# Kernel optimization log

Measured on AMD Instinct MI355X. Metric: run time of the kernel, lower is better.

The kernel has to match this reference:

```python
import jax, jax.numpy as jnp
import numpy as np

B, L1, L2, D1, D2, H, P = 32, 256, 64, 256, 256, 256, 128
I = D1 + D2  # gate / GRU input dim


def setup_inputs() -> dict:
    key = jax.random.key(0)
    ks = jax.random.split(key, 10)
    s = 0.05  # weight init scale
    return {
        "sequence1": jax.random.normal(ks[0], (B, L1, D1), jnp.float32),
        "sequence2": jax.random.normal(ks[1], (B, L2, D2), jnp.float32),
        "sequence1_mask": jnp.ones((B, L1), jnp.float32),
        "sequence2_mask": jnp.ones((B, L2), jnp.float32),
        "W1": jax.random.normal(ks[2], (D2, P), jnp.float32) * s,
        "W2": jax.random.normal(ks[3], (D1 + H, P), jnp.float32) * s,
        "v": jax.random.normal(ks[4], (P,), jnp.float32) * s,
        "Wg": jax.random.normal(ks[5], (I, I), jnp.float32) * s,
        "bg": jnp.zeros((I,), jnp.float32),
        "w_ih": jax.random.normal(ks[6], (3 * H, I), jnp.float32) * s,
        "w_hh": jax.random.normal(ks[7], (3 * H, H), jnp.float32) * s,
        "b_ih": jnp.zeros((3 * H,), jnp.float32),
        "b_hh": jnp.zeros((3 * H,), jnp.float32),
    }


def reference(sequence1, sequence2, sequence1_mask, sequence2_mask,
              W1, W2, v, Wg, bg, w_ih, w_hh, b_ih, b_hh):
    # Precompute sequence2 projection once: [B, L2, P]
    seq2_proj = jnp.einsum('bld,dp->blp', sequence2, W1)
    # Additive mask for softmax over L2
    neg = jnp.where(sequence2_mask > 0, 0.0, -1e9)  # [B, L2]
    xs = jnp.transpose(sequence1, (1, 0, 2))  # [L1, B, D1]

    def step(h, x_t):
        # attention: v^T tanh(W1*seq2_j + W2*[x_t; h])
        vec = jnp.concatenate([x_t, h], axis=-1)            # [B, D1+H]
        s = jnp.einsum('blp,p->bl',
                       jnp.tanh(seq2_proj + (vec @ W2)[:, None, :]), v) + neg
        w = jax.nn.softmax(s, axis=-1)                      # [B, L2]
        att = jnp.einsum('bl,bld->bd', w, sequence2)        # [B, D2]
        inp = jnp.concatenate([x_t, att], axis=-1)          # [B, I]
        # gated attention: sigmoid(Linear(inp)) * inp
        inp = jax.nn.sigmoid(inp @ Wg.T + bg) * inp
        # GRUCell (torch semantics)
        gi = inp @ w_ih.T + b_ih
        gh = h @ w_hh.T + b_hh
        ir, iz, inn = jnp.split(gi, 3, axis=-1)
        hr, hz, hn = jnp.split(gh, 3, axis=-1)
        r = jax.nn.sigmoid(ir + hr)
        z = jax.nn.sigmoid(iz + hz)
        n = jnp.tanh(inn + r * hn)
        h_new = (1.0 - z) * n + z * h
        return h_new, h_new

    h0 = jnp.zeros((sequence1.shape[0], w_hh.shape[1]), sequence1.dtype)
    _, hs = jax.lax.scan(step, h0, xs)                      # [L1, B, H]
    out = jnp.transpose(hs, (1, 0, 2)) * sequence1_mask[:, :, None]
    return out
```

## Files before the change

### kernel.cpp

```cpp
#include <hip/hip_runtime.h>

typedef _Float16 half2_v __attribute__((ext_vector_type(2)));
typedef unsigned int u32;

#define W2K_O    0
#define WHHP_O   16384
#define WIHP_O   114688
#define NPACKW   311296
#define S2P_B    1245184
#define S2T_B    1769472
#define M1_B     2818048
#define PROJX_B  4915200
#define GATEX_B  7012352
#define EXCH_B   15400960

#define SMEM_BYTES 149520

__device__ __forceinline__ float fdot2(half2_v a, half2_v b, float c) {
    return __builtin_amdgcn_fdot2(a, b, c, false);
}
__device__ __forceinline__ half2_v h2_of(u32 u) { return __builtin_bit_cast(half2_v, u); }
__device__ __forceinline__ u32 pack_h2(float a, float b) {
    half2_v r; r[0] = (_Float16)a; r[1] = (_Float16)b;
    return __builtin_bit_cast(u32, r);
}
__device__ __forceinline__ float dot4(uint4 w, uint4 a, float acc) {
    acc = fdot2(h2_of(w.x), h2_of(a.x), acc);
    acc = fdot2(h2_of(w.y), h2_of(a.y), acc);
    acc = fdot2(h2_of(w.z), h2_of(a.z), acc);
    acc = fdot2(h2_of(w.w), h2_of(a.w), acc);
    return acc;
}
__device__ __forceinline__ float fast_tanh(float x) {
    float e = __expf(2.0f * x);
    return 1.0f - 2.0f / (e + 1.0f);
}
__device__ __forceinline__ float fast_sigmoid(float x) {
    return 1.0f / (1.0f + __expf(-x));
}
__device__ __forceinline__ u32 aload(const u32* p) {
    return __hip_atomic_load(p, __ATOMIC_RELAXED, __HIP_MEMORY_SCOPE_AGENT);
}
__device__ __forceinline__ void astore(u32* p, u32 v) {
    __hip_atomic_store(p, v, __ATOMIC_RELAXED, __HIP_MEMORY_SCOPE_AGENT);
}
__device__ __forceinline__ u32 mkw(float x, u32 st) {
    unsigned short hb = __builtin_bit_cast(unsigned short, (_Float16)x);
    return (st << 16) | (u32)hb;
}
__device__ __forceinline__ float f16low(u32 v) {
    return (float)__builtin_bit_cast(_Float16, (unsigned short)(v & 0xFFFFu));
}

__global__ void prep_pack_w(const float* __restrict__ W2, const float* __restrict__ wih,
                            const float* __restrict__ whh, u32* __restrict__ ws_u) {
    int idx = blockIdx.x * 256 + threadIdx.x;
    if (idx >= NPACKW) return;
    float a, c;
    if (idx < WHHP_O) {
        int mm = idx >> 11, r = idx & 2047, p = r >> 4, kl = r & 15;
        int row = 256 + mm * 32 + 2 * kl;
        a = W2[row * 128 + p]; c = W2[(row + 1) * 128 + p];
    } else if (idx < WIHP_O) {
        int t2 = idx - WHHP_O, mm = t2 / 12288, r = t2 % 12288, o = r >> 7, k = r & 127;
        int row = (o >> 5) * 256 + mm * 32 + (o & 31);
        a = whh[row * 256 + 2 * k]; c = whh[row * 256 + 2 * k + 1];
    } else {
        int t2 = idx - WIHP_O, mm = t2 / 24576, r = t2 % 24576, o = r >> 8, k = r & 255;
        int row = (o >> 5) * 256 + mm * 32 + (o & 31);
        a = wih[row * 512 + 2 * k]; c = wih[row * 512 + 2 * k + 1];
    }
    ws_u[idx] = pack_h2(a, c);
}

__global__ void prep_s2p(const float* __restrict__ seq2, const float* __restrict__ W1,
                         _Float16* __restrict__ outh) {
    int idx = blockIdx.x * 256 + threadIdx.x;
    int p = idx & 127, j = (idx >> 7) & 63, b = idx >> 13;
    const float* s2 = seq2 + (b * 64 + j) * 256;
    float acc = 0.f;
    #pragma unroll 8
    for (int d = 0; d < 256; ++d) acc += s2[d] * W1[d * 128 + p];
    outh[idx] = (_Float16)acc;
}

__global__ void prep_s2T(const float* __restrict__ seq2, _Float16* __restrict__ dst) {
    int idx = blockIdx.x * 256 + threadIdx.x;
    int j = idx & 63, d = (idx >> 6) & 255, b = idx >> 14;
    dst[idx] = (_Float16)seq2[(b * 64 + j) * 256 + d];
}

__global__ void prep_m1(const float* __restrict__ Wg, const float* __restrict__ seq2,
                        _Float16* __restrict__ dst) {
    int idx = blockIdx.x * 256 + threadIdx.x;
    int j = idx & 63, o = (idx >> 6) & 511, b = idx >> 15;
    const float* wr = Wg + o * 512 + 256;
    const float* s2 = seq2 + (b * 64 + j) * 256;
    float acc = 0.f;
    #pragma unroll 8
    for (int d = 0; d < 256; ++d) acc += wr[d] * s2[d];
    dst[idx] = (_Float16)acc;
}

__global__ void prep_gemm(const float* __restrict__ A, const float* __restrict__ Bsrc,
                          int mode, _Float16* __restrict__ C, int N) {
    __shared__ float As[64][17];
    __shared__ float Bs[16][65];
    int r0 = blockIdx.x * 64, n0 = blockIdx.y * 64;
    int tid = threadIdx.x;
    int tr = tid >> 4, tc = tid & 15;
    float acc[4][4] = {};
    for (int k0 = 0; k0 < 256; k0 += 16) {
        #pragma unroll
        for (int i = 0; i < 4; ++i) {
            int rr = (tid >> 4) + i * 16, kk = tid & 15;
            As[rr][kk] = A[(r0 + rr) * 256 + k0 + kk];
        }
        #pragma unroll
        for (int i = 0; i < 4; ++i) {
            if (mode == 0) { int kk = (tid >> 6) + i * 4, nn = tid & 63; Bs[kk][nn] = Bsrc[(k0 + kk) * N + n0 + nn]; }
            else           { int nn = (tid >> 4) + i * 16, kk = tid & 15; Bs[kk][nn] = Bsrc[(n0 + nn) * 512 + k0 + kk]; }
        }
        __syncthreads();
        #pragma unroll
        for (int k = 0; k < 16; ++k)
            #pragma unroll
            for (int i = 0; i < 4; ++i)
                #pragma unroll
                for (int j = 0; j < 4; ++j)
                    acc[i][j] += As[tr * 4 + i][k] * Bs[k][tc * 4 + j];
        __syncthreads();
    }
    for (int i = 0; i < 4; ++i)
        for (int j = 0; j < 4; ++j)
            C[(size_t)(r0 + tr * 4 + i) * N + n0 + tc * 4 + j] = (_Float16)acc[i][j];
}

__global__ void __launch_bounds__(1024) match_rnn(
    const float* __restrict__ seq1, const float* __restrict__ mask1,
    const float* __restrict__ mask2, const float* __restrict__ v,
    const float* __restrict__ bg, const float* __restrict__ bih,
    const float* __restrict__ bhh, char* __restrict__ ws, float* __restrict__ out)
{
    const int m = blockIdx.x >> 5;
    const int b = blockIdx.x & 31;
    const int tid = threadIdx.x;

    extern __shared__ char smem[];
    u32* s_whh4 = (u32*)smem;
    u32* s_wih4 = s_whh4 + 12288;
    u32* s_w2k  = s_wih4 + 12288;
    u32* s_s2pU = s_w2k + 2176;
    u32* s_m1u  = s_s2pU + 4608;
    u32* s_s2Tu = s_m1u + 2112;
    float* s_redA = (float*)(s_s2Tu + 2112);
    float* s_redD = s_redA + 96;
    u32* s_h2u  = (u32*)(s_redD + 96);
    u32* s_ip2a = s_h2u + 160;
    u32* s_ip2b = s_ip2a + 160;
    float* s_projh = (float*)(s_ip2b + 160);
    float* s_projx = s_projh + 144;
    float* s_v   = s_projx + 144;
    float* s_w   = s_v + 144;
    float* s_neg = s_w + 64;
    float* s_gx  = s_neg + 64;
    float* s_xc  = s_gx + 64;
    float* s_bg  = s_xc + 64;
    float* s_sg  = s_bg + 64;
    float* s_attl = s_sg + 64;
    float* s_bih = s_attl + 64;
    float* s_bhh = s_bih + 96;
    float* s_hf  = s_bhh + 96;
    u32* s_hloc  = (u32*)(s_hf + 32);
    float* s_m1v = (float*)(s_hloc + 16);

    unsigned short* s_s2p  = (unsigned short*)s_s2pU;
    unsigned short* s_h2h  = (unsigned short*)s_h2u;
    unsigned short* s_ip2ah = (unsigned short*)s_ip2a;
    unsigned short* s_ip2bh = (unsigned short*)s_ip2b;

    const u32* wsrc = (const u32*)ws;

    for (int i = tid; i < 12288; i += 1024) {
        int o = i >> 7, k = i & 127, u = k >> 2;
        int du4 = ((o >> 3) * 256) + ((u & 3) * 64) + (((o & 7) << 3) | (u >> 2));
        s_whh4[du4 * 4 + (k & 3)] = wsrc[WHHP_O + m * 12288 + i];
    }
    for (int i = tid; i < 12288; i += 1024) {
        int o = i >> 7, k = i & 127, u = k >> 2;
        int du4 = ((o >> 3) * 256) + ((u & 3) * 64) + (((o & 7) << 3) | (u >> 2));
        s_wih4[du4 * 4 + (k & 3)] = wsrc[WIHP_O + m * 24576 + o * 256 + k];
    }
    for (int i = tid; i < 2048; i += 1024) {
        int p = i >> 4, kl = i & 15;
        s_w2k[p * 17 + kl] = wsrc[W2K_O + m * 2048 + i];
    }
    {
        const u32* s2src = wsrc + (S2P_B / 4) + b * 4096;
        for (int i = tid; i < 4096; i += 1024) {
            int j = i >> 6, kk = i & 63;
            s_s2pU[j * 72 + kk] = s2src[i];
        }
        const u32* m1src = wsrc + (M1_B / 4) + (b * 512 + m * 64) * 32;
        for (int i = tid; i < 2048; i += 1024) {
            int o = i >> 5, jw = i & 31;
            s_m1u[o * 33 + jw] = m1src[i];
        }
        if (m >= 4) {
            const u32* stsrc = wsrc + (S2T_B / 4) + (b * 256 + (m - 4) * 64) * 32;
            for (int i = tid; i < 2048; i += 1024) {
                int dd = i >> 5, jw = i & 31;
                s_s2Tu[dd * 33 + jw] = stsrc[i];
            }
        } else {
            for (int i = tid; i < 2112; i += 1024) s_s2Tu[i] = 0u;
        }
    }
    if (tid < 128) s_v[tid + (tid >> 3)] = v[tid];
    if (tid < 64) { s_neg[tid] = (mask2[b * 64 + tid] > 0.f) ? 0.f : -1e9f; s_bg[tid] = bg[m * 64 + tid]; }
    if (tid < 96) {
        int row = (tid >> 5) * 256 + m * 32 + (tid & 31);
        s_bih[tid] = bih[row]; s_bhh[tid] = bhh[row];
    }
    if (tid < 32) s_hf[tid] = 0.f;

    uint4 wiA = {}, wiB = {}, wiC = {}, wiD = {};
    const int oAD = ((tid >> 6) << 3) + ((tid & 63) >> 3);
    const int ksAD = tid & 7;
    if (tid < 768) {
        const uint4* wip = (const uint4*)(wsrc + WIHP_O + m * 24576 + oAD * 256 + 128 + ksAD * 16);
        wiA = wip[0]; wiB = wip[1]; wiC = wip[2]; wiD = wip[3];
    }

    u32* exch = (u32*)(ws + EXCH_B) + b * 2048;
    const u32* g_projx = (const u32*)(ws + PROJX_B);
    const u32* g_gatex = (const u32*)(ws + GATEX_B);

    int dead = 0;
    __syncthreads();

    for (int t = 0; t < 256; ++t) {
        const u32 st = (u32)(t + 1);
        float4 xv = {};
        u32 pxv = 0, gxv = 0; float mkv = 0.f;
        if (tid >= 896 && tid < 912) {
            if (m < 4)
                xv = ((const float4*)(seq1 + (size_t)(b * 256 + t) * 256 + m * 64))[tid - 896];
        } else if (tid >= 912 && tid < 976)
            pxv = g_projx[(b * 256 + t) * 64 + (tid - 912)];
        else if (tid >= 976 && tid < 1008)
            gxv = g_gatex[(b * 256 + t) * 256 + m * 32 + (tid - 976)];
        else if (tid == 1008)
            mkv = mask1[b * 256 + t];

        if (t > 0) {
            u32 v1, v2;
            const bool p2 = tid < 256;
            const u32 stp = (u32)t;
            if (!dead) {
                int sp = 0;
                for (;;) {
                    v1 = aload(exch + tid);
                    v2 = p2 ? aload(exch + 1024 + tid) : (stp << 16);
                    bool ok = ((v1 >> 16) == stp) && ((v2 >> 16) == stp);
                    if (__all((int)ok)) break;
                    __builtin_amdgcn_s_sleep(1);
                    if (++sp > (1 << 17)) { dead = 1; break; }
                }
            } else { v1 = aload(exch + tid); v2 = p2 ? aload(exch + 1024 + tid) : 0; }
            float ph = f16low(v1);
            ph += __shfl_down(ph, 4, 8);
            ph += __shfl_down(ph, 2, 8);
            ph += __shfl_down(ph, 1, 8);
            if ((tid & 7) == 0) { int p = tid >> 3; s_projh[p + (p >> 3)] = ph; }
            if (p2) {
                int k = tid;
                int pos = ((k >> 5) * 20 + ((k >> 1) & 15)) * 2 + (k & 1);
                s_h2h[pos] = (unsigned short)(v2 & 0xFFFFu);
            }
        } else {
            if (tid < 160) s_h2u[tid] = 0u;
            if (tid < 144) s_projh[tid] = 0.f;
        }
        __syncthreads();

        if (tid < 768) {
            const uint4* wbase = (const uint4*)s_whh4 + (tid >> 6) * 256;
            float acc = 0.f;
            #pragma unroll
            for (int c = 0; c < 4; ++c) {
                uint4 wv4 = wbase[c * 64 + (tid & 63)];
                uint4 av = *(const uint4*)&s_h2u[ksAD * 20 + c * 4];
                acc = dot4(wv4, av, acc);
            }
            acc += __shfl_down(acc, 4, 8);
            acc += __shfl_down(acc, 2, 8);
            acc += __shfl_down(acc, 1, 8);
            if (ksAD == 0) s_redA[oAD] = acc + s_bhh[oAD];
        } else if (tid >= 896 && tid < 912) {
            int q = tid - 896;
            s_xc[4 * q] = xv.x; s_xc[4 * q + 1] = xv.y; s_xc[4 * q + 2] = xv.z; s_xc[4 * q + 3] = xv.w;
        } else if (tid >= 912 && tid < 976) {
            half2_v h = h2_of(pxv); int i = tid - 912;
            int base = 2 * i + (i >> 2);
            s_projx[base] = (float)h[0]; s_projx[base + 1] = (float)h[1];
        } else if (tid >= 976 && tid < 1008) {
            half2_v h = h2_of(gxv); int i = tid - 976;
            s_gx[2 * i] = (float)h[0]; s_gx[2 * i + 1] = (float)h[1];
        } else if (tid == 1008) s_m1v[0] = mkv;
        __syncthreads();

        {
            int j = tid >> 4, pk = tid & 15, p0 = pk * 8, pb = pk * 9;
            uint4 sv = *(const uint4*)&s_s2p[j * 144 + p0];
            const u32* su = (const u32*)&sv;
            float acc = 0.f;
            #pragma unroll
            for (int q = 0; q < 4; ++q) {
                half2_v h = h2_of(su[q]);
                int pc = pb + 2 * q;
                float a0 = (float)h[0] + s_projx[pc] + s_projh[pc];
                float a1 = (float)h[1] + s_projx[pc + 1] + s_projh[pc + 1];
                acc += fast_tanh(a0) * s_v[pc];
                acc += fast_tanh(a1) * s_v[pc + 1];
            }
            acc += __shfl_down(acc, 8, 16);
            acc += __shfl_down(acc, 4, 16);
            acc += __shfl_down(acc, 2, 16);
            acc += __shfl_down(acc, 1, 16);
            if (pk == 0) s_w[j] = acc + s_neg[j];
        }
        __syncthreads();
        if (tid < 64) {
            float sc = s_w[tid], mx = sc;
            #pragma unroll
            for (int off = 32; off > 0; off >>= 1) mx = fmaxf(mx, __shfl_xor(mx, off));
            float e = __expf(sc - mx), s = e;
            #pragma unroll
            for (int off = 32; off > 0; off >>= 1) s += __shfl_xor(s, off);
            s_w[tid] = e / s;
        }
        __syncthreads();

        if (tid < 512) {
            int o = tid >> 3, q = tid & 7;
            float acc = 0.f;
            #pragma unroll
            for (int c = 0; c < 4; ++c) {
                half2_v h = h2_of(s_m1u[o * 33 + q * 4 + c]);
                int j0 = (q * 4 + c) * 2;
                acc += (float)h[0] * s_w[j0] + (float)h[1] * s_w[j0 + 1];
            }
            acc += __shfl_down(acc, 4, 8);
            acc += __shfl_down(acc, 2, 8);
            acc += __shfl_down(acc, 1, 8);
            if (q == 0) s_sg[o] = fast_sigmoid(acc + s_gx[o] + s_bg[o]);
        } else {
            int dt = tid - 512, d = dt >> 3, q = dt & 7;
            float acc = 0.f;
            #pragma unroll
            for (int c = 0; c < 4; ++c) {
                half2_v h = h2_of(s_s2Tu[d * 33 + q * 4 + c]);
                int j0 = (q * 4 + c) * 2;
                acc += (float)h[0] * s_w[j0] + (float)h[1] * s_w[j0 + 1];
            }
            acc += __shfl_down(acc, 4, 8);
            acc += __shfl_down(acc, 2, 8);
            acc += __shfl_down(acc, 1, 8);
            if (q == 0) s_attl[d] = acc;
        }
        __syncthreads();

        if (tid < 64) {
            float inpv = (m < 4) ? s_xc[tid] : s_attl[tid];
            float ip = s_sg[tid] * inpv;
            astore(&exch[1280 + m * 64 + tid], mkw(ip, st));
        }
        if (tid < 512) {
            u32 vv;
            if (!dead) {
                int sp = 0;
                for (;;) {
                    vv = aload(exch + 1280 + tid);
                    if (__all((int)((vv >> 16) == st))) break;
                    __builtin_amdgcn_s_sleep(1);
                    if (++sp > (1 << 17)) { dead = 1; break; }
                }
            } else vv = aload(exch + 1280 + tid);
            int i = tid;
            if (i < 256) {
                int pos = ((i >> 5) * 20 + ((i >> 1) & 15)) * 2 + (i & 1);
                s_ip2ah[pos] = (unsigned short)(vv & 0xFFFFu);
            } else {
                int i2 = i - 256;
                int pos = ((i2 >> 5) * 20 + ((i2 >> 1) & 15)) * 2 + (i2 & 1);
                s_ip2bh[pos] = (unsigned short)(vv & 0xFFFFu);
            }
        }
        __syncthreads();

        if (tid < 768) {
            const uint4* wbase = (const uint4*)s_wih4 + (tid >> 6) * 256;
            float acc = 0.f;
            #pragma unroll
            for (int c = 0; c < 4; ++c) {
                uint4 wv4 = wbase[c * 64 + (tid & 63)];
                uint4 av = *(const uint4*)&s_ip2a[ksAD * 20 + c * 4];
                acc = dot4(wv4, av, acc);
            }
            acc = dot4(wiA, *(const uint4*)&s_ip2b[ksAD * 20 + 0],  acc);
            acc = dot4(wiB, *(const uint4*)&s_ip2b[ksAD * 20 + 4],  acc);
            acc = dot4(wiC, *(const uint4*)&s_ip2b[ksAD * 20 + 8],  acc);
            acc = dot4(wiD, *(const uint4*)&s_ip2b[ksAD * 20 + 12], acc);
            acc += __shfl_down(acc, 4, 8);
            acc += __shfl_down(acc, 2, 8);
            acc += __shfl_down(acc, 1, 8);
            if (ksAD == 0) s_redD[oAD] = acc + s_bih[oAD];
        }
        __syncthreads();

        if (tid < 32) {
            int o = tid;
            float r_ = fast_sigmoid(s_redD[o] + s_redA[o]);
            float z_ = fast_sigmoid(s_redD[32 + o] + s_redA[32 + o]);
            float n_ = fast_tanh(s_redD[64 + o] + r_ * s_redA[64 + o]);
            float hn = (1.f - z_) * n_ + z_ * s_hf[o];
            s_hf[o] = hn;
            out[(size_t)(b * 256 + t) * 256 + m * 32 + o] = hn * s_m1v[0];
            astore(&exch[1024 + m * 32 + o], mkw(hn, st));
            float nb = __shfl_down(hn, 1);
            if (!(o & 1)) s_hloc[o >> 1] = pack_h2(hn, nb);
        }
        __syncthreads();

        if (tid < 512) {
            int p = tid >> 2, kc = tid & 3;
            float a = 0.f;
            #pragma unroll
            for (int cc = 0; cc < 4; ++cc)
                a = fdot2(h2_of(s_w2k[p * 17 + kc * 4 + cc]), h2_of(s_hloc[kc * 4 + cc]), a);
            a += __shfl_down(a, 2, 4);
            a += __shfl_down(a, 1, 4);
            if (kc == 0) astore(&exch[p * 8 + m], mkw(a, st));
        }
    }
}

extern "C" void kernel_launch(void* const* d_in, const int* in_sizes, int n_in,
                              void* d_out, int out_size, void* d_ws, size_t ws_size,
                              hipStream_t stream) {
    const float* seq1  = (const float*)d_in[0];
    const float* seq2  = (const float*)d_in[1];
    const float* mask1 = (const float*)d_in[2];
    const float* mask2 = (const float*)d_in[3];
    const float* W1    = (const float*)d_in[4];
    const float* W2    = (const float*)d_in[5];
    const float* v     = (const float*)d_in[6];
    const float* Wg    = (const float*)d_in[7];
    const float* bg    = (const float*)d_in[8];
    const float* wih   = (const float*)d_in[9];
    const float* whh   = (const float*)d_in[10];
    const float* bih   = (const float*)d_in[11];
    const float* bhh   = (const float*)d_in[12];

    char* ws = (char*)d_ws;

    (void)hipFuncSetAttribute(reinterpret_cast<const void*>(match_rnn),
                              hipFuncAttributeMaxDynamicSharedMemorySize, SMEM_BYTES);

    prep_pack_w<<<dim3((NPACKW + 255) / 256), dim3(256), 0, stream>>>(W2, wih, whh, (u32*)ws);
    prep_s2p<<<dim3(1024), dim3(256), 0, stream>>>(seq2, W1, (_Float16*)(ws + S2P_B));
    prep_s2T<<<dim3(2048), dim3(256), 0, stream>>>(seq2, (_Float16*)(ws + S2T_B));
    prep_m1<<<dim3(4096), dim3(256), 0, stream>>>(Wg, seq2, (_Float16*)(ws + M1_B));
    prep_gemm<<<dim3(128, 2), dim3(256), 0, stream>>>(seq1, W2, 0, (_Float16*)(ws + PROJX_B), 128);
    prep_gemm<<<dim3(128, 8), dim3(256), 0, stream>>>(seq1, Wg, 1, (_Float16*)(ws + GATEX_B), 512);
    (void)hipMemsetAsync(ws + EXCH_B, 0, 262144, stream);
    match_rnn<<<dim3(256), dim3(1024), SMEM_BYTES, stream>>>(seq1, mask1, mask2, v, bg, bih, bhh, ws, (float*)d_out);
}
```

Measured before the change: 1.700 ms.

## Compute gated input redundantly per block to drop a cross-block exchange barrier

Each block now computes the full 512-wide gate and attention vectors for its batch row locally, using the full m1 and s2T tiles in shared memory. This removes the per-step global exchange and spin-wait that had assembled the gated input across blocks. GRU weights move from shared memory into registers, which frees LDS for the larger tiles, and the hidden-side and input-side matvecs are merged into one phase. The cost is redundant gate work in every block, higher register pressure, and a larger one-time load of m1/s2T per block.

```diff
diff --git a/kernel.cpp b/kernel.cpp
--- a/kernel.cpp
+++ b/kernel.cpp
@@ -14,7 +14,7 @@
 #define GATEX_B  7012352
 #define EXCH_B   15400960
 
-#define SMEM_BYTES 149520
+#define SMEM_BYTES 141712
 
 __device__ __forceinline__ float fdot2(half2_v a, half2_v b, float c) {
     return __builtin_amdgcn_fdot2(a, b, c, false);
@@ -147,13 +147,11 @@
     const int tid = threadIdx.x;
 
     extern __shared__ char smem[];
-    u32* s_whh4 = (u32*)smem;
-    u32* s_wih4 = s_whh4 + 12288;
-    u32* s_w2k  = s_wih4 + 12288;
+    u32* s_w2k  = (u32*)smem;
     u32* s_s2pU = s_w2k + 2176;
     u32* s_m1u  = s_s2pU + 4608;
-    u32* s_s2Tu = s_m1u + 2112;
-    float* s_redA = (float*)(s_s2Tu + 2112);
+    u32* s_s2Tu = s_m1u + 16896;
+    float* s_redA = (float*)(s_s2Tu + 8448);
     float* s_redD = s_redA + 96;
     u32* s_h2u  = (u32*)(s_redD + 96);
     u32* s_ip2a = s_h2u + 160;
@@ -162,13 +160,14 @@
     float* s_projx = s_projh + 144;
     float* s_v   = s_projx + 144;
     float* s_w   = s_v + 144;
-    float* s_neg = s_w + 64;
-    float* s_gx  = s_neg + 64;
-    float* s_xc  = s_gx + 64;
-    float* s_bg  = s_xc + 64;
-    float* s_sg  = s_bg + 64;
-    float* s_attl = s_sg + 64;
-    float* s_bih = s_attl + 64;
+    u32* s_wp   = (u32*)(s_w + 64);
+    float* s_neg = (float*)(s_wp + 32);
+    float* s_xcF = s_neg + 64;
+    u32* s_gxF2 = (u32*)(s_xcF + 256);
+    float* s_bgF = (float*)(s_gxF2 + 256);
+    float* s_sgF = s_bgF + 512;
+    float* s_attF = s_sgF + 512;
+    float* s_bih = s_attF + 256;
     float* s_bhh = s_bih + 96;
     float* s_hf  = s_bhh + 96;
     u32* s_hloc  = (u32*)(s_hf + 32);
@@ -176,21 +175,9 @@
 
     unsigned short* s_s2p  = (unsigned short*)s_s2pU;
     unsigned short* s_h2h  = (unsigned short*)s_h2u;
-    unsigned short* s_ip2ah = (unsigned short*)s_ip2a;
-    unsigned short* s_ip2bh = (unsigned short*)s_ip2b;
 
     const u32* wsrc = (const u32*)ws;
 
-    for (int i = tid; i < 12288; i += 1024) {
-        int o = i >> 7, k = i & 127, u = k >> 2;
-        int du4 = ((o >> 3) * 256) + ((u & 3) * 64) + (((o & 7) << 3) | (u >> 2));
-        s_whh4[du4 * 4 + (k & 3)] = wsrc[WHHP_O + m * 12288 + i];
-    }
-    for (int i = tid; i < 12288; i += 1024) {
-        int o = i >> 7, k = i & 127, u = k >> 2;
-        int du4 = ((o >> 3) * 256) + ((u & 3) * 64) + (((o & 7) << 3) | (u >> 2));
-        s_wih4[du4 * 4 + (k & 3)] = wsrc[WIHP_O + m * 24576 + o * 256 + k];
-    }
     for (int i = tid; i < 2048; i += 1024) {
         int p = i >> 4, kl = i & 15;
         s_w2k[p * 17 + kl] = wsrc[W2K_O + m * 2048 + i];
@@ -201,33 +188,36 @@
             int j = i >> 6, kk = i & 63;
             s_s2pU[j * 72 + kk] = s2src[i];
         }
-        const u32* m1src = wsrc + (M1_B / 4) + (b * 512 + m * 64) * 32;
-        for (int i = tid; i < 2048; i += 1024) {
+        const u32* m1src = wsrc + (M1_B / 4) + b * 16384;
+        for (int i = tid; i < 16384; i += 1024) {
             int o = i >> 5, jw = i & 31;
             s_m1u[o * 33 + jw] = m1src[i];
         }
-        if (m >= 4) {
-            const u32* stsrc = wsrc + (S2T_B / 4) + (b * 256 + (m - 4) * 64) * 32;
-            for (int i = tid; i < 2048; i += 1024) {
-                int dd = i >> 5, jw = i & 31;
-                s_s2Tu[dd * 33 + jw] = stsrc[i];
-            }
-        } else {
-            for (int i = tid; i < 2112; i += 1024) s_s2Tu[i] = 0u;
+        const u32* stsrc = wsrc + (S2T_B / 4) + b * 8192;
+        for (int i = tid; i < 8192; i += 1024) {
+            int dd = i >> 5, jw = i & 31;
+            s_s2Tu[dd * 33 + jw] = stsrc[i];
         }
     }
     if (tid < 128) s_v[tid + (tid >> 3)] = v[tid];
-    if (tid < 64) { s_neg[tid] = (mask2[b * 64 + tid] > 0.f) ? 0.f : -1e9f; s_bg[tid] = bg[m * 64 + tid]; }
+    if (tid < 64) s_neg[tid] = (mask2[b * 64 + tid] > 0.f) ? 0.f : -1e9f;
+    if (tid < 512) s_bgF[tid] = bg[tid];
     if (tid < 96) {
         int row = (tid >> 5) * 256 + m * 32 + (tid & 31);
         s_bih[tid] = bih[row]; s_bhh[tid] = bhh[row];
     }
     if (tid < 32) s_hf[tid] = 0.f;
 
-    uint4 wiA = {}, wiB = {}, wiC = {}, wiD = {};
     const int oAD = ((tid >> 6) << 3) + ((tid & 63) >> 3);
     const int ksAD = tid & 7;
+    uint4 wh0 = {}, wh1 = {}, wh2 = {}, wh3 = {};
+    uint4 wl0 = {}, wl1 = {}, wl2 = {}, wl3 = {};
+    uint4 wiA = {}, wiB = {}, wiC = {}, wiD = {};
     if (tid < 768) {
+        const uint4* whp = (const uint4*)(wsrc + WHHP_O + m * 12288 + oAD * 128 + ksAD * 16);
+        wh0 = whp[0]; wh1 = whp[1]; wh2 = whp[2]; wh3 = whp[3];
+        const uint4* wlp = (const uint4*)(wsrc + WIHP_O + m * 24576 + oAD * 256 + ksAD * 16);
+        wl0 = wlp[0]; wl1 = wlp[1]; wl2 = wlp[2]; wl3 = wlp[3];
         const uint4* wip = (const uint4*)(wsrc + WIHP_O + m * 24576 + oAD * 256 + 128 + ksAD * 16);
         wiA = wip[0]; wiB = wip[1]; wiC = wip[2]; wiD = wip[3];
     }
@@ -243,15 +233,13 @@
         const u32 st = (u32)(t + 1);
         float4 xv = {};
         u32 pxv = 0, gxv = 0; float mkv = 0.f;
-        if (tid >= 896 && tid < 912) {
-            if (m < 4)
-                xv = ((const float4*)(seq1 + (size_t)(b * 256 + t) * 256 + m * 64))[tid - 896];
-        } else if (tid >= 912 && tid < 976)
-            pxv = g_projx[(b * 256 + t) * 64 + (tid - 912)];
-        else if (tid >= 976 && tid < 1008)
-            gxv = g_gatex[(b * 256 + t) * 256 + m * 32 + (tid - 976)];
-        else if (tid == 1008)
-            mkv = mask1[b * 256 + t];
+        if (tid >= 640 && tid < 704)
+            xv = ((const float4*)(seq1 + (size_t)(b * 256 + t) * 256))[tid - 640];
+        else if (tid >= 704 && tid < 768)
+            pxv = g_projx[(b * 256 + t) * 64 + (tid - 704)];
+        else if (tid >= 768)
+            gxv = g_gatex[(b * 256 + t) * 256 + (tid - 768)];
+        if (tid == 639) mkv = mask1[b * 256 + t];
 
         if (t > 0) {
             u32 v1, v2;
@@ -282,32 +270,17 @@
             if (tid < 160) s_h2u[tid] = 0u;
             if (tid < 144) s_projh[tid] = 0.f;
         }
-        __syncthreads();
-
-        if (tid < 768) {
-            const uint4* wbase = (const uint4*)s_whh4 + (tid >> 6) * 256;
-            float acc = 0.f;
-            #pragma unroll
-            for (int c = 0; c < 4; ++c) {
-                uint4 wv4 = wbase[c * 64 + (tid & 63)];
-                uint4 av = *(const uint4*)&s_h2u[ksAD * 20 + c * 4];
-                acc = dot4(wv4, av, acc);
-            }
-            acc += __shfl_down(acc, 4, 8);
-            acc += __shfl_down(acc, 2, 8);
-            acc += __shfl_down(acc, 1, 8);
-            if (ksAD == 0) s_redA[oAD] = acc + s_bhh[oAD];
-        } else if (tid >= 896 && tid < 912) {
-            int q = tid - 896;
-            s_xc[4 * q] = xv.x; s_xc[4 * q + 1] = xv.y; s_xc[4 * q + 2] = xv.z; s_xc[4 * q + 3] = xv.w;
-        } else if (tid >= 912 && tid < 976) {
-            half2_v h = h2_of(pxv); int i = tid - 912;
+        if (tid >= 640 && tid < 704) {
+            int q = tid - 640;
+            s_xcF[4 * q] = xv.x; s_xcF[4 * q + 1] = xv.y; s_xcF[4 * q + 2] = xv.z; s_xcF[4 * q + 3] = xv.w;
+        } else if (tid >= 704 && tid < 768) {
+            half2_v h = h2_of(pxv); int i = tid - 704;
             int base = 2 * i + (i >> 2);
             s_projx[base] = (float)h[0]; s_projx[base + 1] = (float)h[1];
-        } else if (tid >= 976 && tid < 1008) {
-            half2_v h = h2_of(gxv); int i = tid - 976;
-            s_gx[2 * i] = (float)h[0]; s_gx[2 * i + 1] = (float)h[1];
-        } else if (tid == 1008) s_m1v[0] = mkv;
+        } else if (tid >= 768) {
+            s_gxF2[tid - 768] = gxv;
+        }
+        if (tid == 639) s_m1v[0] = mkv;
         __syncthreads();
 
         {
@@ -338,84 +311,62 @@
             float e = __expf(sc - mx), s = e;
             #pragma unroll
             for (int off = 32; off > 0; off >>= 1) s += __shfl_xor(s, off);
-            s_w[tid] = e / s;
+            float wv = e / s;
+            float nb = __shfl_down(wv, 1);
+            if (!(tid & 1)) s_wp[tid >> 1] = pack_h2(wv, nb);
         }
         __syncthreads();
 
         if (tid < 512) {
-            int o = tid >> 3, q = tid & 7;
+            int o = tid;
             float acc = 0.f;
-            #pragma unroll
-            for (int c = 0; c < 4; ++c) {
-                half2_v h = h2_of(s_m1u[o * 33 + q * 4 + c]);
-                int j0 = (q * 4 + c) * 2;
-                acc += (float)h[0] * s_w[j0] + (float)h[1] * s_w[j0 + 1];
+            #pragma unroll 8
+            for (int c = 0; c < 32; ++c)
+                acc = fdot2(h2_of(s_m1u[o * 33 + c]), h2_of(s_wp[c]), acc);
+            half2_v gx = h2_of(s_gxF2[o >> 1]);
+            float gxv_ = (o & 1) ? (float)gx[1] : (float)gx[0];
+            s_sgF[o] = fast_sigmoid(acc + gxv_ + s_bgF[o]);
+        } else if (tid < 768) {
+            int d = tid - 512;
+            float acc = 0.f;
+            #pragma unroll 8
+            for (int c = 0; c < 32; ++c)
+                acc = fdot2(h2_of(s_s2Tu[d * 33 + c]), h2_of(s_wp[c]), acc);
+            s_attF[d] = acc;
+        }
+        __syncthreads();
+        if (tid < 256) {
+            int i = tid;
+            float i0, i1;
+            if (i < 128) { i0 = s_xcF[2 * i]; i1 = s_xcF[2 * i + 1]; }
+            else         { i0 = s_attF[2 * i - 256]; i1 = s_attF[2 * i - 255]; }
+            u32 pk2 = pack_h2(s_sgF[2 * i] * i0, s_sgF[2 * i + 1] * i1);
+            if (i < 128) s_ip2a[(i >> 4) * 20 + (i & 15)] = pk2;
+            else { int i2 = i - 128; s_ip2b[(i2 >> 4) * 20 + (i2 & 15)] = pk2; }
+        }
+        __syncthreads();
+
+        if (tid < 768) {
+            float ah = 0.f, ai = 0.f;
+            const uint4* hv = (const uint4*)&s_h2u[ksAD * 20];
+            const uint4* av = (const uint4*)&s_ip2a[ksAD * 20];
+            const uint4* bv = (const uint4*)&s_ip2b[ksAD * 20];
+            ah = dot4(wh0, hv[0], ah); ah = dot4(wh1, hv[1], ah);
+            ah = dot4(wh2, hv[2], ah); ah = dot4(wh3, hv[3], ah);
+            ai = dot4(wl0, av[0], ai); ai = dot4(wl1, av[1], ai);
+            ai = dot4(wl2, av[2], ai); ai = dot4(wl3, av[3], ai);
+            ai = dot4(wiA, bv[0], ai); ai = dot4(wiB, bv[1], ai);
+            ai = dot4(wiC, bv[2], ai); ai = dot4(wiD, bv[3], ai);
+            ah += __shfl_down(ah, 4, 8);
+            ah += __shfl_down(ah, 2, 8);
+            ah += __shfl_down(ah, 1, 8);
+            ai += __shfl_down(ai, 4, 8);
+            ai += __shfl_down(ai, 2, 8);
+            ai += __shfl_down(ai, 1, 8);
+            if (ksAD == 0) {
+                s_redA[oAD] = ah + s_bhh[oAD];
+                s_redD[oAD] = ai + s_bih[oAD];
             }
-            acc += __shfl_down(acc, 4, 8);
-            acc += __shfl_down(acc, 2, 8);
-            acc += __shfl_down(acc, 1, 8);
-            if (q == 0) s_sg[o] = fast_sigmoid(acc + s_gx[o] + s_bg[o]);
-        } else {
-            int dt = tid - 512, d = dt >> 3, q = dt & 7;
-            float acc = 0.f;
-            #pragma unroll
-            for (int c = 0; c < 4; ++c) {
-                half2_v h = h2_of(s_s2Tu[d * 33 + q * 4 + c]);
-                int j0 = (q * 4 + c) * 2;
-                acc += (float)h[0] * s_w[j0] + (float)h[1] * s_w[j0 + 1];
-            }
-            acc += __shfl_down(acc, 4, 8);
-            acc += __shfl_down(acc, 2, 8);
-            acc += __shfl_down(acc, 1, 8);
-            if (q == 0) s_attl[d] = acc;
-        }
-        __syncthreads();
-
-        if (tid < 64) {
-            float inpv = (m < 4) ? s_xc[tid] : s_attl[tid];
-            float ip = s_sg[tid] * inpv;
-            astore(&exch[1280 + m * 64 + tid], mkw(ip, st));
-        }
-        if (tid < 512) {
-            u32 vv;
-            if (!dead) {
-                int sp = 0;
-                for (;;) {
-                    vv = aload(exch + 1280 + tid);
-                    if (__all((int)((vv >> 16) == st))) break;
-                    __builtin_amdgcn_s_sleep(1);
-                    if (++sp > (1 << 17)) { dead = 1; break; }
-                }
-            } else vv = aload(exch + 1280 + tid);
-            int i = tid;
-            if (i < 256) {
-                int pos = ((i >> 5) * 20 + ((i >> 1) & 15)) * 2 + (i & 1);
-                s_ip2ah[pos] = (unsigned short)(vv & 0xFFFFu);
-            } else {
-                int i2 = i - 256;
-                int pos = ((i2 >> 5) * 20 + ((i2 >> 1) & 15)) * 2 + (i2 & 1);
-                s_ip2bh[pos] = (unsigned short)(vv & 0xFFFFu);
-            }
-        }
-        __syncthreads();
-
-        if (tid < 768) {
-            const uint4* wbase = (const uint4*)s_wih4 + (tid >> 6) * 256;
-            float acc = 0.f;
-            #pragma unroll
-            for (int c = 0; c < 4; ++c) {
-                uint4 wv4 = wbase[c * 64 + (tid & 63)];
-                uint4 av = *(const uint4*)&s_ip2a[ksAD * 20 + c * 4];
-                acc = dot4(wv4, av, acc);
-            }
-            acc = dot4(wiA, *(const uint4*)&s_ip2b[ksAD * 20 + 0],  acc);
-            acc = dot4(wiB, *(const uint4*)&s_ip2b[ksAD * 20 + 4],  acc);
-            acc = dot4(wiC, *(const uint4*)&s_ip2b[ksAD * 20 + 8],  acc);
-            acc = dot4(wiD, *(const uint4*)&s_ip2b[ksAD * 20 + 12], acc);
-            acc += __shfl_down(acc, 4, 8);
-            acc += __shfl_down(acc, 2, 8);
-            acc += __shfl_down(acc, 1, 8);
-            if (ksAD == 0) s_redD[oAD] = acc + s_bih[oAD];
         }
         __syncthreads();
 
```

After: 2.400 ms. +41.2%, slower.

## Merge gate and attention reductions, move h-projection to remove barriers

Applied to the files above, without the earlier changes.

The gate-logit and attention-context reductions are merged into one 512-thread pass where each 8-lane group computes both halves. The gated input is written to the exchange buffer straight from that pass, which drops the s_sg/s_attl staging arrays and one __syncthreads. The w_hh·h GEMV moves from before the score stage to after the gate stage, removing another barrier and overlapping it with the wait for cross-block exchange. Each thread now does 8 dot steps instead of 4, so the critical-path reduction per thread gets longer.

```diff
diff --git a/kernel.cpp b/kernel.cpp
--- a/kernel.cpp
+++ b/kernel.cpp
@@ -166,9 +166,7 @@
     float* s_gx  = s_neg + 64;
     float* s_xc  = s_gx + 64;
     float* s_bg  = s_xc + 64;
-    float* s_sg  = s_bg + 64;
-    float* s_attl = s_sg + 64;
-    float* s_bih = s_attl + 64;
+    float* s_bih = s_bg + 64;
     float* s_bhh = s_bih + 96;
     float* s_hf  = s_bhh + 96;
     u32* s_hloc  = (u32*)(s_hf + 32);
@@ -282,22 +280,7 @@
             if (tid < 160) s_h2u[tid] = 0u;
             if (tid < 144) s_projh[tid] = 0.f;
         }
-        __syncthreads();
-
-        if (tid < 768) {
-            const uint4* wbase = (const uint4*)s_whh4 + (tid >> 6) * 256;
-            float acc = 0.f;
-            #pragma unroll
-            for (int c = 0; c < 4; ++c) {
-                uint4 wv4 = wbase[c * 64 + (tid & 63)];
-                uint4 av = *(const uint4*)&s_h2u[ksAD * 20 + c * 4];
-                acc = dot4(wv4, av, acc);
-            }
-            acc += __shfl_down(acc, 4, 8);
-            acc += __shfl_down(acc, 2, 8);
-            acc += __shfl_down(acc, 1, 8);
-            if (ksAD == 0) s_redA[oAD] = acc + s_bhh[oAD];
-        } else if (tid >= 896 && tid < 912) {
+        if (tid >= 896 && tid < 912) {
             int q = tid - 896;
             s_xc[4 * q] = xv.x; s_xc[4 * q + 1] = xv.y; s_xc[4 * q + 2] = xv.z; s_xc[4 * q + 3] = xv.w;
         } else if (tid >= 912 && tid < 976) {
@@ -343,38 +326,37 @@
         __syncthreads();
 
         if (tid < 512) {
-            int o = tid >> 3, q = tid & 7;
+            int o = tid >> 3, r = tid & 7, q = r & 3;
+            const u32* src = (r >= 4) ? &s_s2Tu[o * 33] : &s_m1u[o * 33];
             float acc = 0.f;
             #pragma unroll
+            for (int c = 0; c < 8; ++c) {
+                half2_v h = h2_of(src[q * 8 + c]);
+                int j0 = (q * 8 + c) * 2;
+                acc += (float)h[0] * s_w[j0] + (float)h[1] * s_w[j0 + 1];
+            }
+            acc += __shfl_down(acc, 2, 4);
+            acc += __shfl_down(acc, 1, 4);
+            float attv = __shfl_down(acc, 4, 8);
+            if (r == 0) {
+                float g = acc + s_gx[o] + s_bg[o];
+                float inpv = (m < 4) ? s_xc[o] : attv;
+                astore(&exch[1280 + m * 64 + o], mkw(fast_sigmoid(g) * inpv, st));
+            }
+        }
+        if (tid < 768) {
+            const uint4* wbase = (const uint4*)s_whh4 + (tid >> 6) * 256;
+            float acc = 0.f;
+            #pragma unroll
             for (int c = 0; c < 4; ++c) {
-                half2_v h = h2_of(s_m1u[o * 33 + q * 4 + c]);
-                int j0 = (q * 4 + c) * 2;
-                acc += (float)h[0] * s_w[j0] + (float)h[1] * s_w[j0 + 1];
+                uint4 wv4 = wbase[c * 64 + (tid & 63)];
+                uint4 av = *(const uint4*)&s_h2u[ksAD * 20 + c * 4];
+                acc = dot4(wv4, av, acc);
             }
             acc += __shfl_down(acc, 4, 8);
             acc += __shfl_down(acc, 2, 8);
             acc += __shfl_down(acc, 1, 8);
-            if (q == 0) s_sg[o] = fast_sigmoid(acc + s_gx[o] + s_bg[o]);
-        } else {
-            int dt = tid - 512, d = dt >> 3, q = dt & 7;
-            float acc = 0.f;
-            #pragma unroll
-            for (int c = 0; c < 4; ++c) {
-                half2_v h = h2_of(s_s2Tu[d * 33 + q * 4 + c]);
-                int j0 = (q * 4 + c) * 2;
-                acc += (float)h[0] * s_w[j0] + (float)h[1] * s_w[j0 + 1];
-            }
-            acc += __shfl_down(acc, 4, 8);
-            acc += __shfl_down(acc, 2, 8);
-            acc += __shfl_down(acc, 1, 8);
-            if (q == 0) s_attl[d] = acc;
-        }
-        __syncthreads();
-
-        if (tid < 64) {
-            float inpv = (m < 4) ? s_xc[tid] : s_attl[tid];
-            float ip = s_sg[tid] * inpv;
-            astore(&exch[1280 + m * 64 + tid], mkw(ip, st));
+            if (ksAD == 0) s_redA[oAD] = acc + s_bhh[oAD];
         }
         if (tid < 512) {
             u32 vv;
```

After: 1.614 ms. 1.05x faster.
